# Optimization experiments

Hardware: AMD Instinct MI355X
Metric: run time of the kernel (lower is better)

The kernel has to match this reference:

```python
import jax, jax.numpy as jnp
import numpy as np

N = 32768      # total points (8 clouds x 4096)
B = 8          # clouds in batch
D_IN = 64      # input feature dim
M = 8192       # sampled centers (ratio=0.25)
K = 32         # knn neighbors
R = 0.2        # ball radius
DIMS = [D_IN + 3, 128, 128, 256]  # edge MLP (PointNetConv local_nn)


def setup_inputs() -> dict:
    key = jax.random.key(0)
    ks = jax.random.split(key, 10)
    x = jax.random.normal(ks[0], (N, D_IN), jnp.float32)
    pos = jax.random.uniform(ks[1], (N, 3), jnp.float32)  # unit cube
    batch = jnp.repeat(jnp.arange(B, dtype=jnp.int32), N // B)
    # deterministic stand-in for torch.sort(torch.randperm(N)[:M])
    idx = jnp.sort(jax.random.permutation(ks[2], N)[:M]).astype(jnp.int32)
    params = {}
    for i in range(3):
        fan_in = DIMS[i]
        params[f"W{i+1}"] = jax.random.normal(ks[3 + 2 * i], (DIMS[i], DIMS[i + 1]), jnp.float32) / np.sqrt(fan_in)
        params[f"b{i+1}"] = jnp.zeros((DIMS[i + 1],), jnp.float32)
    return {"x": x, "pos": pos, "batch": batch, "idx": idx, **params}


def _knn_ball(pos, batch, idx, k, r):
    """Batched KNN restricted to same cloud, then radius mask (ball query)."""
    centers = pos[idx]                                   # [M, 3]
    d2 = (jnp.sum(centers ** 2, -1)[:, None]
          + jnp.sum(pos ** 2, -1)[None, :]
          - 2.0 * centers @ pos.T)                       # [M, N]
    same = batch[idx][:, None] == batch[None, :]
    d2 = jnp.where(same, d2, jnp.inf)
    neg_d2, nbr = jax.lax.top_k(-d2, k)                  # [M, K]
    valid = (-neg_d2) <= r * r                           # ball-query radius clip
    return nbr, valid


def reference(x, pos, batch, idx, W1, b1, W2, b2, W3, b3):
    nbr, valid = _knn_ball(pos, batch, idx, K, R)        # [M,K], [M,K]
    centers = pos[idx]                                   # [M, 3]
    rel = pos[nbr] - centers[:, None, :]                 # [M, K, 3]
    feat = jnp.concatenate([x[nbr], rel], axis=-1)       # [M, K, D_IN+3]
    h = jax.nn.relu(feat @ W1 + b1)
    h = jax.nn.relu(h @ W2 + b2)
    h = jax.nn.relu(h @ W3 + b3)                         # [M, K, 256]
    # max aggregation over valid neighbors (scatter-max equivalent)
    h = jnp.where(valid[:, :, None], h, -jnp.inf)
    out = jnp.max(h, axis=1)                             # [M, 256]
    return out, pos[idx], batch[idx]
```

## Files before the change

### kernel.cpp

```cpp
#include <hip/hip_runtime.h>


typedef unsigned short u16;
typedef unsigned int u32;
typedef unsigned long long u64;
typedef __bf16 bf16x8 __attribute__((ext_vector_type(8)));
typedef float floatx4 __attribute__((ext_vector_type(4)));

#define PCLOUD 4096
#define DIN    64
#define MCENT  8192
#define KNBR   32
#define CAP    448

#define OFF_LIST  0
#define OFF_HIST  14336
#define OFF_NBRL  14848
#define OFF_CNT   15360
#define OFF_CEN   15392
#define OFF_BCL   15456

__device__ inline u16 f2bf(float f) {
    u32 b = __float_as_uint(f);
    b += 0x7fffu + ((b >> 16) & 1u);
    return (u16)(b >> 16);
}
__device__ inline u32 cvtpk(float a, float b) {
    u32 r;
    asm("v_cvt_pk_bf16_f32 %0, %1, %2" : "=v"(r) : "v"(a), "v"(b));
    return r;
}
__device__ inline u64 wave_min_u64(u64 v) {
    #pragma unroll
    for (int off = 32; off; off >>= 1) {
        u64 o = __shfl_xor((unsigned long long)v, off);
        if (o < v) v = o;
    }
    return v;
}
__device__ inline u64 d2key(float d2, int j) {
    u32 u = __float_as_uint(d2);
    u = (u & 0x80000000u) ? ~u : (u | 0x80000000u);
    return ((u64)u << 32) | (u32)j;
}
__device__ inline int key_bucket(u64 k) {
    u32 hi = (u32)(k >> 32);
    if (hi < 0x80000000u) return 0;
    float d2 = __uint_as_float(hi & 0x7fffffffu);
    int b = (int)(d2 * 800.0f);
    return b > 31 ? 31 : b;
}

__global__ void prep_kernel(const float* __restrict__ W1, const float* __restrict__ W2,
                            const float* __restrict__ W3, uint4* __restrict__ ws) {
    int t = blockIdx.x * 256 + threadIdx.x;
    int g = t >> 11, r = t & 2047;
    int n = r >> 4, kc = r & 15;
    const float* W; int rs, n0, krows;
    if (g == 0)      { W = W1; rs = 128; n0 = 0;   krows = 67;  }
    else if (g == 1) { W = W2; rs = 128; n0 = 0;   krows = 128; }
    else if (g == 2) { W = W3; rs = 256; n0 = 0;   krows = 128; }
    else             { W = W3; rs = 256; n0 = 128; krows = 128; }
    u16 e[8];
    #pragma unroll
    for (int j = 0; j < 8; j++) {
        int k = kc * 8 + j;
        e[j] = (k < krows) ? f2bf(W[(size_t)k * rs + n0 + n]) : (u16)0;
    }
    ws[(g << 11) + (n << 4) + (kc ^ (n & 7))] = *(const uint4*)e;
}

template <bool WS>
__device__ __forceinline__ void commitW(int s, uint4 ld, uint4* __restrict__ buf, int tid,
                                        const float* __restrict__ W1,
                                        const float* __restrict__ W2,
                                        const float* __restrict__ W3) {
    if constexpr (WS) {
        buf[tid] = ld;
    } else {
        const float* W; int rs, n0, krows;
        if (s < 8)       { W = W1; rs = 128; n0 = s * 16;        krows = 67;  }
        else if (s < 16) { W = W2; rs = 128; n0 = (s - 8) * 16;  krows = 128; }
        else             { W = W3; rs = 256; n0 = (s - 16) * 16; krows = 128; }
        int n = tid >> 4, kc = tid & 15;
        u16 e[8];
        #pragma unroll
        for (int j = 0; j < 8; j++) {
            int k = kc * 8 + j;
            e[j] = (k < krows) ? f2bf(W[(size_t)k * rs + n0 + n]) : (u16)0;
        }
        buf[(n << 4) + (kc ^ (n & 7))] = *(const uint4*)e;
    }
}

__device__ __forceinline__ void push_hit(int c, float d2, int j,
                                         int* acnt, u64* lists) {
    int p = atomicAdd(&acnt[c], 1);
    if (p < CAP) lists[c * CAP + p] = d2key(d2, j);
}

template <bool WS>
__global__ __launch_bounds__(256, 4) void sa_kernel(
    const float* __restrict__ x, const float* __restrict__ pos,
    const int* __restrict__ batch, const int* __restrict__ idx,
    const float* __restrict__ W1, const float* __restrict__ b1,
    const float* __restrict__ W2, const float* __restrict__ b2,
    const float* __restrict__ W3, const float* __restrict__ b3,
    const uint4* __restrict__ ws4, float* __restrict__ out) {
    __shared__ __align__(16) char smem[40960];
    u64*  lists = (u64*)(smem + OFF_LIST);
    u32*  hist  = (u32*)(smem + OFF_HIST);
    int*  nbrl  = (int*)(smem + OFF_NBRL);
    int*  acnt  = (int*)(smem + OFF_CNT);
    int*  cnt2  = (int*)(smem + OFF_CNT + 16);
    float4* cen = (float4*)(smem + OFF_CEN);
    int*  bcls  = (int*)(smem + OFF_BCL);

    int tid = threadIdx.x, w = tid >> 6, l = tid & 63;
    int bid = blockIdx.x;
    int m0 = ((bid & 7) << 10) + ((bid >> 3) << 2);
    int m = m0 + w;
    int ic = idx[m] & (8 * PCLOUD - 1);
    float cx = pos[ic * 3], cy = pos[ic * 3 + 1], cz = pos[ic * 3 + 2];
    float sc = __fadd_rn(__fadd_rn(__fmul_rn(cx, cx), __fmul_rn(cy, cy)), __fmul_rn(cz, cz));
    int bcl = batch[ic] & 7;
    int base = bcl << 12;
    const float R2 = 0.04f;

    if (l == 0) { cen[w] = make_float4(cx, cy, cz, sc); bcls[w] = bcl; }
    if (tid < 4) { acnt[tid] = 0; cnt2[tid] = 0; }
    if (l == 1) {
        float* o1 = out + MCENT * 256;
        o1[m * 3] = cx; o1[m * 3 + 1] = cy; o1[m * 3 + 2] = cz;
        (o1 + MCENT * 3)[m] = (float)bcl;
    }
    __syncthreads();

    bool uni = (bcls[0] == bcls[1]) && (bcls[1] == bcls[2]) && (bcls[2] == bcls[3]);
    if (uni) {
        float4 cA = cen[0], cB = cen[1], cC = cen[2], cD = cen[3];
        int jb = bcls[0] << 12;
        const float4* pb4 = (const float4*)(pos + (size_t)jb * 3);

#define TEST1(CEN, CI, SP, PX, PY, PZ, J) { \
    float dt = __fadd_rn(__fadd_rn(__fmul_rn(CEN.x, PX), __fmul_rn(CEN.y, PY)), __fmul_rn(CEN.z, PZ)); \
    float d2 = __fsub_rn(__fadd_rn(CEN.w, SP), __fmul_rn(2.0f, dt)); \
    if (d2 <= R2) push_hit(CI, d2, J, acnt, lists); }
#define TESTP(PX, PY, PZ, J) { \
    float sp = __fadd_rn(__fadd_rn(__fmul_rn(PX, PX), __fmul_rn(PY, PY)), __fmul_rn(PZ, PZ)); \
    TEST1(cA, 0, sp, PX, PY, PZ, J) \
    TEST1(cB, 1, sp, PX, PY, PZ, J) \
    TEST1(cC, 2, sp, PX, PY, PZ, J) \
    TEST1(cD, 3, sp, PX, PY, PZ, J) }

        #pragma unroll
        for (int it = 0; it < 4; it++) {
            int tq = it * 256 + tid;
            float4 q0 = pb4[tq * 3], q1 = pb4[tq * 3 + 1], q2 = pb4[tq * 3 + 2];
            int j0 = jb + tq * 4;
            TESTP(q0.x, q0.y, q0.z, j0)
            TESTP(q0.w, q1.x, q1.y, j0 + 1)
            TESTP(q1.z, q1.w, q2.x, j0 + 2)
            TESTP(q2.y, q2.z, q2.w, j0 + 3)
        }
#undef TESTP
#undef TEST1
    } else {
        for (int t = l; t < PCLOUD; t += 64) {
            int j = base + t;
            float px = pos[j * 3], py = pos[j * 3 + 1], pz = pos[j * 3 + 2];
            float sp = __fadd_rn(__fadd_rn(__fmul_rn(px, px), __fmul_rn(py, py)), __fmul_rn(pz, pz));
            float dt = __fadd_rn(__fadd_rn(__fmul_rn(cx, px), __fmul_rn(cy, py)), __fmul_rn(cz, pz));
            float d2 = __fsub_rn(__fadd_rn(sc, sp), __fmul_rn(2.0f, dt));
            if (d2 <= R2) push_hit(w, d2, j, acnt, lists);
        }
    }
    __syncthreads();

    int c = acnt[w];
    int nsel = c < KNBR ? c : KNBR;
    u64* mylist = lists + w * CAP;

    int selj = -1;
    if (c <= KNBR) {
        if (l < c) selj = (int)(u32)mylist[l];
    } else if (c <= CAP) {
        u64 kk[7];
        int bk[7];
        if (l < 32) hist[w * 32 + l] = 0;
        #pragma unroll
        for (int i = 0; i < 7; i++) kk[i] = (l + i * 64 < c) ? mylist[l + i * 64] : ~0ull;
        #pragma unroll
        for (int i = 0; i < 7; i++) {
            bk[i] = 32;
            if (kk[i] != ~0ull) {
                bk[i] = key_bucket(kk[i]);
                atomicAdd(&hist[w * 32 + bk[i]], 1u);
            }
        }
        int hv = (l < 32) ? (int)hist[w * 32 + l] : 0;
        #pragma unroll
        for (int off = 1; off <= 16; off <<= 1) {
            int o = __shfl_up(hv, off);
            if (l >= off) hv += o;
        }
        u64 ge = __ballot((l < 32) && (hv >= KNBR));
        int B = __ffsll((unsigned long long)ge) - 1;
        int S = (B == 0) ? 0 : __shfl(hv, B - 1);
        #pragma unroll
        for (int i = 0; i < 7; i++) {
            if (kk[i] != ~0ull) {
                if (bk[i] < B) { int p = atomicAdd(&cnt2[w], 1); nbrl[w * 32 + p] = (int)(u32)kk[i]; }
                if (bk[i] != B) kk[i] = ~0ull;
            }
        }
        int need = KNBR - S;
        u64 last = 0;
        for (int r = 0; r < need; r++) {
            u64 mn = ~0ull;
            #pragma unroll
            for (int i = 0; i < 7; i++) if (kk[i] > last && kk[i] < mn) mn = kk[i];
            mn = wave_min_u64(mn);
            if (l == 0) nbrl[w * 32 + S + r] = (int)(u32)mn;
            last = mn;
        }
        if (l < KNBR) selj = nbrl[w * 32 + l];
    } else {
        u64 last = 0;
        for (int r = 0; r < KNBR; r++) {
            u64 mn = ~0ull;
            for (int t = l; t < PCLOUD; t += 64) {
                int j = base + t;
                float px = pos[j * 3], py = pos[j * 3 + 1], pz = pos[j * 3 + 2];
                float sp = __fadd_rn(__fadd_rn(__fmul_rn(px, px), __fmul_rn(py, py)), __fmul_rn(pz, pz));
                float dt = __fadd_rn(__fadd_rn(__fmul_rn(cx, px), __fmul_rn(cy, py)), __fmul_rn(cz, pz));
                float d2 = __fsub_rn(__fadd_rn(sc, sp), __fmul_rn(2.0f, dt));
                if (d2 <= R2) { u64 kf = d2key(d2, j); if (kf > last && kf < mn) mn = kf; }
            }
            mn = wave_min_u64(mn);
            if (l == r) selj = (int)(u32)mn;
            last = mn;
        }
    }
    __syncthreads();

    uint4* sA4  = (uint4*)smem;
    uint4* sWb0 = (uint4*)(smem + 32768);
    uint4* sWb1 = (uint4*)(smem + 36864);

    uint4 ld = {};
    if constexpr (WS) ld = ws4[tid];

    {
        int h = l & 1, rl = l >> 1;
        int row = w * 32 + rl;
        int j = __shfl(selj, rl);
        int xv = row & 7;
        uint4* dst = sA4 + row * 16;
        uint4 z; z.x = z.y = z.z = z.w = 0;
        if (j >= 0) {
            const float4* sx = (const float4*)(x + (size_t)j * DIN);
            int c0lo = h ? 6 : 0, c0hi = h ? 8 : 6;
            for (int c0 = c0lo; c0 < c0hi; c0++) {
                float4 f0 = sx[c0 * 2], f1 = sx[c0 * 2 + 1];
                uint4 pv;
                pv.x = cvtpk(f0.x, f0.y); pv.y = cvtpk(f0.z, f0.w);
                pv.z = cvtpk(f1.x, f1.y); pv.w = cvtpk(f1.z, f1.w);
                dst[c0 ^ xv] = pv;
            }
            if (h == 1) {
                float rx = pos[j * 3] - cx, ry = pos[j * 3 + 1] - cy, rz = pos[j * 3 + 2] - cz;
                uint4 rc; rc.x = cvtpk(rx, ry); rc.y = cvtpk(rz, 0.0f); rc.z = 0; rc.w = 0;
                dst[8 ^ xv] = rc;
                dst[9 ^ xv] = z; dst[10 ^ xv] = z; dst[11 ^ xv] = z;
            }
        } else {
            int c0lo = h ? 6 : 0, c0hi = h ? 12 : 6;
            for (int c0 = c0lo; c0 < c0hi; c0++) dst[c0 ^ xv] = z;
        }
    }
    commitW<WS>(0, ld, sWb0, tid, W1, W2, W3);
    if constexpr (WS) ld = ws4[256 + tid];
    __syncthreads();

    int m16 = l & 15, quad = l >> 4;
    int r0 = w * 32;
    const floatx4 vzero = {0.f, 0.f, 0.f, 0.f};

    {
        bf16x8 a1[3][2];
        #pragma unroll
        for (int ki = 0; ki < 3; ki++)
            #pragma unroll
            for (int t = 0; t < 2; t++) {
                int row = r0 + t * 16 + m16;
                a1[ki][t] = __builtin_bit_cast(bf16x8, sA4[row * 16 + ((ki * 4 + quad) ^ (row & 7))]);
            }
        #pragma unroll 2
        for (int s = 0; s < 8; s++) {
            uint4* buf  = (s & 1) ? sWb1 : sWb0;
            uint4* nbuf = (s & 1) ? sWb0 : sWb1;
            floatx4 acc[2] = {vzero, vzero};
            #pragma unroll
            for (int ki = 0; ki < 3; ki++) {
                bf16x8 b = __builtin_bit_cast(bf16x8, buf[(m16 << 4) + ((ki * 4 + quad) ^ (m16 & 7))]);
                #pragma unroll
                for (int t = 0; t < 2; t++)
                    acc[t] = __builtin_amdgcn_mfma_f32_16x16x32_bf16(b, a1[ki][t], acc[t], 0, 0, 0);
            }
            float4 bb = ((const float4*)b1)[s * 4 + quad];
            #pragma unroll
            for (int t = 0; t < 2; t++) {
                int rr = r0 + t * 16 + m16;
                uint2 pv;
                pv.x = cvtpk(fmaxf(acc[t][0] + bb.x, 0.f), fmaxf(acc[t][1] + bb.y, 0.f));
                pv.y = cvtpk(fmaxf(acc[t][2] + bb.z, 0.f), fmaxf(acc[t][3] + bb.w, 0.f));
                *(uint2*)(smem + rr * 256 + (((s * 2 + (quad >> 1)) ^ (rr & 7)) << 4) + ((quad & 1) << 3)) = pv;
            }
            commitW<WS>(s + 1, ld, nbuf, tid, W1, W2, W3);
            if constexpr (WS) ld = ws4[(s + 2) * 256 + tid];
            __syncthreads();
        }
    }

    {
        bf16x8 a2[4][2];
        #pragma unroll
        for (int ki = 0; ki < 4; ki++)
            #pragma unroll
            for (int t = 0; t < 2; t++) {
                int row = r0 + t * 16 + m16;
                a2[ki][t] = __builtin_bit_cast(bf16x8, sA4[row * 16 + ((ki * 4 + quad) ^ (row & 7))]);
            }
        #pragma unroll 2
        for (int s = 0; s < 8; s++) {
            uint4* buf  = (s & 1) ? sWb1 : sWb0;
            uint4* nbuf = (s & 1) ? sWb0 : sWb1;
            floatx4 acc[2] = {vzero, vzero};
            #pragma unroll
            for (int ki = 0; ki < 4; ki++) {
                bf16x8 b = __builtin_bit_cast(bf16x8, buf[(m16 << 4) + ((ki * 4 + quad) ^ (m16 & 7))]);
                #pragma unroll
                for (int t = 0; t < 2; t++)
                    acc[t] = __builtin_amdgcn_mfma_f32_16x16x32_bf16(b, a2[ki][t], acc[t], 0, 0, 0);
            }
            float4 bb = ((const float4*)b2)[s * 4 + quad];
            #pragma unroll
            for (int t = 0; t < 2; t++) {
                int rr = r0 + t * 16 + m16;
                uint2 pv;
                pv.x = cvtpk(fmaxf(acc[t][0] + bb.x, 0.f), fmaxf(acc[t][1] + bb.y, 0.f));
                pv.y = cvtpk(fmaxf(acc[t][2] + bb.z, 0.f), fmaxf(acc[t][3] + bb.w, 0.f));
                *(uint2*)(smem + rr * 256 + (((s * 2 + (quad >> 1)) ^ (rr & 7)) << 4) + ((quad & 1) << 3)) = pv;
            }
            commitW<WS>(s + 9, ld, nbuf, tid, W1, W2, W3);
            if constexpr (WS) ld = ws4[(s + 10) * 256 + tid];
            __syncthreads();
        }
    }

    {
        bf16x8 a3[4][2];
        #pragma unroll
        for (int ki = 0; ki < 4; ki++)
            #pragma unroll
            for (int t = 0; t < 2; t++) {
                int row = r0 + t * 16 + m16;
                a3[ki][t] = __builtin_bit_cast(bf16x8, sA4[row * 16 + ((ki * 4 + quad) ^ (row & 7))]);
            }
        #pragma unroll 2
        for (int s = 0; s < 16; s++) {
            uint4* buf  = (s & 1) ? sWb1 : sWb0;
            uint4* nbuf = (s & 1) ? sWb0 : sWb1;
            floatx4 acc[2] = {vzero, vzero};
            #pragma unroll
            for (int ki = 0; ki < 4; ki++) {
                bf16x8 b = __builtin_bit_cast(bf16x8, buf[(m16 << 4) + ((ki * 4 + quad) ^ (m16 & 7))]);
                #pragma unroll
                for (int t = 0; t < 2; t++)
                    acc[t] = __builtin_amdgcn_mfma_f32_16x16x32_bf16(a3[ki][t], b, acc[t], 0, 0, 0);
            }
            int col = s * 16 + m16;
            float bias = b3[col];
            float mv = 0.0f;
            #pragma unroll
            for (int t = 0; t < 2; t++)
                #pragma unroll
                for (int i = 0; i < 4; i++) {
                    int k = t * 16 + quad * 4 + i;
                    float v = fmaxf(acc[t][i] + bias, 0.0f);
                    if (k < nsel) mv = fmaxf(mv, v);
                }
            mv = fmaxf(mv, __shfl_xor(mv, 16));
            mv = fmaxf(mv, __shfl_xor(mv, 32));
            if (quad == 0) out[(m0 + w) * 256 + col] = mv;
            if (s < 15) {
                commitW<WS>(s + 17, ld, nbuf, tid, W1, W2, W3);
                if constexpr (WS) { if (s < 14) ld = ws4[(s + 18) * 256 + tid]; }
                __syncthreads();
            }
        }
    }
}

extern "C" void kernel_launch(void* const* d_in, const int* in_sizes, int n_in,
                              void* d_out, int out_size, void* d_ws, size_t ws_size,
                              hipStream_t stream) {
    const float* x     = (const float*)d_in[0];
    const float* pos   = (const float*)d_in[1];
    const int*   batch = (const int*)d_in[2];
    const int*   idx   = (const int*)d_in[3];
    const float* W1    = (const float*)d_in[4];
    const float* b1    = (const float*)d_in[5];
    const float* W2    = (const float*)d_in[6];
    const float* b2    = (const float*)d_in[7];
    const float* W3    = (const float*)d_in[8];
    const float* b3    = (const float*)d_in[9];
    float* out = (float*)d_out;
    uint4* ws4 = (uint4*)d_ws;

    if (ws_size >= 131072) {
        hipLaunchKernelGGL(prep_kernel, dim3(32), dim3(256), 0, stream, W1, W2, W3, ws4);
        hipLaunchKernelGGL((sa_kernel<true>), dim3(MCENT / 4), dim3(256), 0, stream,
                           x, pos, batch, idx, W1, b1, W2, b2, W3, b3, ws4, out);
    } else {
        hipLaunchKernelGGL((sa_kernel<false>), dim3(MCENT / 4), dim3(256), 0, stream,
                           x, pos, batch, idx, W1, b1, W2, b2, W3, b3, ws4, out);
    }
}
```

Before: 152.1 us.

## Stream weights in 32-column slabs and prefetch first slab during KNN

Weight staging buffers are doubled so each pipeline stage covers 32 output columns instead of 16, which halves the number of barrier-separated stages across the three MLP layers. The first weight slab is loaded and committed to shared memory before the neighbor search, so its latency overlaps the KNN phase. MFMA sections are wrapped in s_setprio raises. Shared memory grows to 48 KB and launch bounds drop from 4 to 3 blocks per CU, trading occupancy for fewer syncs.

Result: slower. 170.3 us (+11.9%).

```diff
diff --git a/kernel.cpp b/kernel.cpp
--- a/kernel.cpp
+++ b/kernel.cpp
@@ -71,25 +71,31 @@
 }
 
 template <bool WS>
-__device__ __forceinline__ void commitW(int s, uint4 ld, uint4* __restrict__ buf, int tid,
-                                        const float* __restrict__ W1,
-                                        const float* __restrict__ W2,
-                                        const float* __restrict__ W3) {
+__device__ __forceinline__ void commitW32(int g, uint4 ld0, uint4 ld1,
+                                          uint4* __restrict__ buf, int tid,
+                                          const float* __restrict__ W1,
+                                          const float* __restrict__ W2,
+                                          const float* __restrict__ W3) {
     if constexpr (WS) {
-        buf[tid] = ld;
+        buf[tid] = ld0;
+        buf[256 + tid] = ld1;
     } else {
-        const float* W; int rs, n0, krows;
-        if (s < 8)       { W = W1; rs = 128; n0 = s * 16;        krows = 67;  }
-        else if (s < 16) { W = W2; rs = 128; n0 = (s - 8) * 16;  krows = 128; }
-        else             { W = W3; rs = 256; n0 = (s - 16) * 16; krows = 128; }
-        int n = tid >> 4, kc = tid & 15;
-        u16 e[8];
-        #pragma unroll
-        for (int j = 0; j < 8; j++) {
-            int k = kc * 8 + j;
-            e[j] = (k < krows) ? f2bf(W[(size_t)k * rs + n0 + n]) : (u16)0;
-        }
-        buf[(n << 4) + (kc ^ (n & 7))] = *(const uint4*)e;
+        #pragma unroll
+        for (int h = 0; h < 2; h++) {
+            int b = g * 2 + h;
+            const float* W; int rs, n0, krows;
+            if (b < 8)       { W = W1; rs = 128; n0 = b * 16;        krows = 67;  }
+            else if (b < 16) { W = W2; rs = 128; n0 = (b - 8) * 16;  krows = 128; }
+            else             { W = W3; rs = 256; n0 = (b - 16) * 16; krows = 128; }
+            int n = tid >> 4, kc = tid & 15;
+            u16 e[8];
+            #pragma unroll
+            for (int j = 0; j < 8; j++) {
+                int k = kc * 8 + j;
+                e[j] = (k < krows) ? f2bf(W[(size_t)k * rs + n0 + n]) : (u16)0;
+            }
+            buf[h * 256 + (n << 4) + (kc ^ (n & 7))] = *(const uint4*)e;
+        }
     }
 }
 
@@ -100,14 +106,14 @@
 }
 
 template <bool WS>
-__global__ __launch_bounds__(256, 4) void sa_kernel(
+__global__ __launch_bounds__(256, 3) void sa_kernel(
     const float* __restrict__ x, const float* __restrict__ pos,
     const int* __restrict__ batch, const int* __restrict__ idx,
     const float* __restrict__ W1, const float* __restrict__ b1,
     const float* __restrict__ W2, const float* __restrict__ b2,
     const float* __restrict__ W3, const float* __restrict__ b3,
     const uint4* __restrict__ ws4, float* __restrict__ out) {
-    __shared__ __align__(16) char smem[40960];
+    __shared__ __align__(16) char smem[49152];
     u64*  lists = (u64*)(smem + OFF_LIST);
     u32*  hist  = (u32*)(smem + OFF_HIST);
     int*  nbrl  = (int*)(smem + OFF_NBRL);
@@ -116,7 +122,14 @@
     float4* cen = (float4*)(smem + OFF_CEN);
     int*  bcls  = (int*)(smem + OFF_BCL);
 
+    uint4* sA4  = (uint4*)smem;
+    uint4* sWb0 = (uint4*)(smem + 32768);
+    uint4* sWb1 = (uint4*)(smem + 40960);
+
     int tid = threadIdx.x, w = tid >> 6, l = tid & 63;
+    uint4 ld0 = {}, ld1 = {};
+    if constexpr (WS) { ld0 = ws4[tid]; ld1 = ws4[256 + tid]; }
+
     int bid = blockIdx.x;
     int m0 = ((bid & 7) << 10) + ((bid >> 3) << 2);
     int m = m0 + w;
@@ -134,6 +147,7 @@
         o1[m * 3] = cx; o1[m * 3 + 1] = cy; o1[m * 3 + 2] = cz;
         (o1 + MCENT * 3)[m] = (float)bcl;
     }
+    commitW32<WS>(0, ld0, ld1, sWb0, tid, W1, W2, W3);
     __syncthreads();
 
     bool uni = (bcls[0] == bcls[1]) && (bcls[1] == bcls[2]) && (bcls[2] == bcls[3]);
@@ -244,12 +258,7 @@
     }
     __syncthreads();
 
-    uint4* sA4  = (uint4*)smem;
-    uint4* sWb0 = (uint4*)(smem + 32768);
-    uint4* sWb1 = (uint4*)(smem + 36864);
-
-    uint4 ld = {};
-    if constexpr (WS) ld = ws4[tid];
+    if constexpr (WS) { ld0 = ws4[512 + tid]; ld1 = ws4[768 + tid]; }
 
     {
         int h = l & 1, rl = l >> 1;
@@ -279,8 +288,6 @@
             for (int c0 = c0lo; c0 < c0hi; c0++) dst[c0 ^ xv] = z;
         }
     }
-    commitW<WS>(0, ld, sWb0, tid, W1, W2, W3);
-    if constexpr (WS) ld = ws4[256 + tid];
     __syncthreads();
 
     int m16 = l & 15, quad = l >> 4;
@@ -295,108 +302,139 @@
             for (int t = 0; t < 2; t++) {
                 int row = r0 + t * 16 + m16;
                 a1[ki][t] = __builtin_bit_cast(bf16x8, sA4[row * 16 + ((ki * 4 + quad) ^ (row & 7))]);
+            }
+        #pragma unroll 2
+        for (int s = 0; s < 4; s++) {
+            uint4* buf  = (s & 1) ? sWb1 : sWb0;
+            uint4* nbuf = (s & 1) ? sWb0 : sWb1;
+            floatx4 acc[2][2] = {{vzero, vzero}, {vzero, vzero}};
+            __builtin_amdgcn_s_setprio(1);
+            #pragma unroll
+            for (int ki = 0; ki < 3; ki++) {
+                int cb = ki * 4 + quad;
+                #pragma unroll
+                for (int cc = 0; cc < 2; cc++) {
+                    bf16x8 b = __builtin_bit_cast(bf16x8, buf[cc * 256 + (m16 << 4) + (cb ^ (m16 & 7))]);
+                    #pragma unroll
+                    for (int t = 0; t < 2; t++)
+                        acc[t][cc] = __builtin_amdgcn_mfma_f32_16x16x32_bf16(b, a1[ki][t], acc[t][cc], 0, 0, 0);
+                }
+            }
+            __builtin_amdgcn_s_setprio(0);
+            #pragma unroll
+            for (int t = 0; t < 2; t++) {
+                int rr = r0 + t * 16 + m16;
+                #pragma unroll
+                for (int cc = 0; cc < 2; cc++) {
+                    float4 bb = ((const float4*)b1)[s * 8 + cc * 4 + quad];
+                    uint2 pv;
+                    pv.x = cvtpk(fmaxf(acc[t][cc][0] + bb.x, 0.f), fmaxf(acc[t][cc][1] + bb.y, 0.f));
+                    pv.y = cvtpk(fmaxf(acc[t][cc][2] + bb.z, 0.f), fmaxf(acc[t][cc][3] + bb.w, 0.f));
+                    *(uint2*)(smem + rr * 256 + (((s * 4 + cc * 2 + (quad >> 1)) ^ (rr & 7)) << 4)
+                              + ((quad & 1) << 3)) = pv;
+                }
+            }
+            commitW32<WS>(s + 1, ld0, ld1, nbuf, tid, W1, W2, W3);
+            if constexpr (WS) { ld0 = ws4[(s + 2) * 512 + tid]; ld1 = ws4[(s + 2) * 512 + 256 + tid]; }
+            __syncthreads();
+        }
+    }
+
+    {
+        bf16x8 a2[4][2];
+        #pragma unroll
+        for (int ki = 0; ki < 4; ki++)
+            #pragma unroll
+            for (int t = 0; t < 2; t++) {
+                int row = r0 + t * 16 + m16;
+                a2[ki][t] = __builtin_bit_cast(bf16x8, sA4[row * 16 + ((ki * 4 + quad) ^ (row & 7))]);
+            }
+        #pragma unroll 2
+        for (int s = 0; s < 4; s++) {
+            uint4* buf  = (s & 1) ? sWb1 : sWb0;
+            uint4* nbuf = (s & 1) ? sWb0 : sWb1;
+            floatx4 acc[2][2] = {{vzero, vzero}, {vzero, vzero}};
+            __builtin_amdgcn_s_setprio(1);
+            #pragma unroll
+            for (int ki = 0; ki < 4; ki++) {
+                int cb = ki * 4 + quad;
+                #pragma unroll
+                for (int cc = 0; cc < 2; cc++) {
+                    bf16x8 b = __builtin_bit_cast(bf16x8, buf[cc * 256 + (m16 << 4) + (cb ^ (m16 & 7))]);
+                    #pragma unroll
+                    for (int t = 0; t < 2; t++)
+                        acc[t][cc] = __builtin_amdgcn_mfma_f32_16x16x32_bf16(b, a2[ki][t], acc[t][cc], 0, 0, 0);
+                }
+            }
+            __builtin_amdgcn_s_setprio(0);
+            #pragma unroll
+            for (int t = 0; t < 2; t++) {
+                int rr = r0 + t * 16 + m16;
+                #pragma unroll
+                for (int cc = 0; cc < 2; cc++) {
+                    float4 bb = ((const float4*)b2)[s * 8 + cc * 4 + quad];
+                    uint2 pv;
+                    pv.x = cvtpk(fmaxf(acc[t][cc][0] + bb.x, 0.f), fmaxf(acc[t][cc][1] + bb.y, 0.f));
+                    pv.y = cvtpk(fmaxf(acc[t][cc][2] + bb.z, 0.f), fmaxf(acc[t][cc][3] + bb.w, 0.f));
+                    *(uint2*)(smem + rr * 256 + (((s * 4 + cc * 2 + (quad >> 1)) ^ (rr & 7)) << 4)
+                              + ((quad & 1) << 3)) = pv;
+                }
+            }
+            commitW32<WS>(s + 5, ld0, ld1, nbuf, tid, W1, W2, W3);
+            if constexpr (WS) { ld0 = ws4[(s + 6) * 512 + tid]; ld1 = ws4[(s + 6) * 512 + 256 + tid]; }
+            __syncthreads();
+        }
+    }
+
+    {
+        bf16x8 a3[4][2];
+        #pragma unroll
+        for (int ki = 0; ki < 4; ki++)
+            #pragma unroll
+            for (int t = 0; t < 2; t++) {
+                int row = r0 + t * 16 + m16;
+                a3[ki][t] = __builtin_bit_cast(bf16x8, sA4[row * 16 + ((ki * 4 + quad) ^ (row & 7))]);
             }
         #pragma unroll 2
         for (int s = 0; s < 8; s++) {
             uint4* buf  = (s & 1) ? sWb1 : sWb0;
             uint4* nbuf = (s & 1) ? sWb0 : sWb1;
-            floatx4 acc[2] = {vzero, vzero};
-            #pragma unroll
-            for (int ki = 0; ki < 3; ki++) {
-                bf16x8 b = __builtin_bit_cast(bf16x8, buf[(m16 << 4) + ((ki * 4 + quad) ^ (m16 & 7))]);
+            floatx4 acc[2][2] = {{vzero, vzero}, {vzero, vzero}};
+            __builtin_amdgcn_s_setprio(1);
+            #pragma unroll
+            for (int ki = 0; ki < 4; ki++) {
+                int cb = ki * 4 + quad;
+                #pragma unroll
+                for (int cc = 0; cc < 2; cc++) {
+                    bf16x8 b = __builtin_bit_cast(bf16x8, buf[cc * 256 + (m16 << 4) + (cb ^ (m16 & 7))]);
+                    #pragma unroll
+                    for (int t = 0; t < 2; t++)
+                        acc[t][cc] = __builtin_amdgcn_mfma_f32_16x16x32_bf16(a3[ki][t], b, acc[t][cc], 0, 0, 0);
+                }
+            }
+            __builtin_amdgcn_s_setprio(0);
+            #pragma unroll
+            for (int cc = 0; cc < 2; cc++) {
+                int col = s * 32 + cc * 16 + m16;
+                float bias = b3[col];
+                float mv = 0.0f;
                 #pragma unroll
                 for (int t = 0; t < 2; t++)
-                    acc[t] = __builtin_amdgcn_mfma_f32_16x16x32_bf16(b, a1[ki][t], acc[t], 0, 0, 0);
-            }
-            float4 bb = ((const float4*)b1)[s * 4 + quad];
-            #pragma unroll
-            for (int t = 0; t < 2; t++) {
-                int rr = r0 + t * 16 + m16;
-                uint2 pv;
-                pv.x = cvtpk(fmaxf(acc[t][0] + bb.x, 0.f), fmaxf(acc[t][1] + bb.y, 0.f));
-                pv.y = cvtpk(fmaxf(acc[t][2] + bb.z, 0.f), fmaxf(acc[t][3] + bb.w, 0.f));
-                *(uint2*)(smem + rr * 256 + (((s * 2 + (quad >> 1)) ^ (rr & 7)) << 4) + ((quad & 1) << 3)) = pv;
-            }
-            commitW<WS>(s + 1, ld, nbuf, tid, W1, W2, W3);
-            if constexpr (WS) ld = ws4[(s + 2) * 256 + tid];
-            __syncthreads();
-        }
-    }
-
-    {
-        bf16x8 a2[4][2];
-        #pragma unroll
-        for (int ki = 0; ki < 4; ki++)
-            #pragma unroll
-            for (int t = 0; t < 2; t++) {
-                int row = r0 + t * 16 + m16;
-                a2[ki][t] = __builtin_bit_cast(bf16x8, sA4[row * 16 + ((ki * 4 + quad) ^ (row & 7))]);
-            }
-        #pragma unroll 2
-        for (int s = 0; s < 8; s++) {
-            uint4* buf  = (s & 1) ? sWb1 : sWb0;
-            uint4* nbuf = (s & 1) ? sWb0 : sWb1;
-            floatx4 acc[2] = {vzero, vzero};
-            #pragma unroll
-            for (int ki = 0; ki < 4; ki++) {
-                bf16x8 b = __builtin_bit_cast(bf16x8, buf[(m16 << 4) + ((ki * 4 + quad) ^ (m16 & 7))]);
-                #pragma unroll
-                for (int t = 0; t < 2; t++)
-                    acc[t] = __builtin_amdgcn_mfma_f32_16x16x32_bf16(b, a2[ki][t], acc[t], 0, 0, 0);
-            }
-            float4 bb = ((const float4*)b2)[s * 4 + quad];
-            #pragma unroll
-            for (int t = 0; t < 2; t++) {
-                int rr = r0 + t * 16 + m16;
-                uint2 pv;
-                pv.x = cvtpk(fmaxf(acc[t][0] + bb.x, 0.f), fmaxf(acc[t][1] + bb.y, 0.f));
-                pv.y = cvtpk(fmaxf(acc[t][2] + bb.z, 0.f), fmaxf(acc[t][3] + bb.w, 0.f));
-                *(uint2*)(smem + rr * 256 + (((s * 2 + (quad >> 1)) ^ (rr & 7)) << 4) + ((quad & 1) << 3)) = pv;
-            }
-            commitW<WS>(s + 9, ld, nbuf, tid, W1, W2, W3);
-            if constexpr (WS) ld = ws4[(s + 10) * 256 + tid];
-            __syncthreads();
-        }
-    }
-
-    {
-        bf16x8 a3[4][2];
-        #pragma unroll
-        for (int ki = 0; ki < 4; ki++)
-            #pragma unroll
-            for (int t = 0; t < 2; t++) {
-                int row = r0 + t * 16 + m16;
-                a3[ki][t] = __builtin_bit_cast(bf16x8, sA4[row * 16 + ((ki * 4 + quad) ^ (row & 7))]);
-            }
-        #pragma unroll 2
-        for (int s = 0; s < 16; s++) {
-            uint4* buf  = (s & 1) ? sWb1 : sWb0;
-            uint4* nbuf = (s & 1) ? sWb0 : sWb1;
-            floatx4 acc[2] = {vzero, vzero};
-            #pragma unroll
-            for (int ki = 0; ki < 4; ki++) {
-                bf16x8 b = __builtin_bit_cast(bf16x8, buf[(m16 << 4) + ((ki * 4 + quad) ^ (m16 & 7))]);
-                #pragma unroll
-                for (int t = 0; t < 2; t++)
-                    acc[t] = __builtin_amdgcn_mfma_f32_16x16x32_bf16(a3[ki][t], b, acc[t], 0, 0, 0);
-            }
-            int col = s * 16 + m16;
-            float bias = b3[col];
-            float mv = 0.0f;
-            #pragma unroll
-            for (int t = 0; t < 2; t++)
-                #pragma unroll
-                for (int i = 0; i < 4; i++) {
-                    int k = t * 16 + quad * 4 + i;
-                    float v = fmaxf(acc[t][i] + bias, 0.0f);
-                    if (k < nsel) mv = fmaxf(mv, v);
-                }
-            mv = fmaxf(mv, __shfl_xor(mv, 16));
-            mv = fmaxf(mv, __shfl_xor(mv, 32));
-            if (quad == 0) out[(m0 + w) * 256 + col] = mv;
-            if (s < 15) {
-                commitW<WS>(s + 17, ld, nbuf, tid, W1, W2, W3);
-                if constexpr (WS) { if (s < 14) ld = ws4[(s + 18) * 256 + tid]; }
+                    #pragma unroll
+                    for (int i = 0; i < 4; i++) {
+                        int k = t * 16 + quad * 4 + i;
+                        float v = fmaxf(acc[t][cc][i] + bias, 0.0f);
+                        if (k < nsel) mv = fmaxf(mv, v);
+                    }
+                mv = fmaxf(mv, __shfl_xor(mv, 16));
+                mv = fmaxf(mv, __shfl_xor(mv, 32));
+                if (quad == 0) out[(m0 + w) * 256 + col] = mv;
+            }
+            if (s < 7) {
+                commitW32<WS>(s + 9, ld0, ld1, nbuf, tid, W1, W2, W3);
+                if constexpr (WS) {
+                    if (s < 6) { ld0 = ws4[(s + 10) * 512 + tid]; ld1 = ws4[(s + 10) * 512 + 256 + tid]; }
+                }
                 __syncthreads();
             }
         }
```

## Load MLP weight fragments directly into registers and drop block barriers

Applied to the files above, without the earlier changes.

Replaces the LDS double-buffered weight staging, written by all 256 threads and fenced by __syncthreads every step, with per-wave register prefetch. Each wave now reads its B fragments straight from the pre-swizzled workspace, or converts them from fp32 in the fallback path, one column block ahead. This removes the block-wide barriers between MLP steps and cuts shared memory from 40 KB to 32 KB. MFMA sections are wrapped in s_setprio. The cost is that every wave fetches the full weight set from cache, so L2 traffic rises about fourfold, and full unrolling adds register pressure.

Measured after the change: 163.7 us. +7.6%, slower.

```diff
diff --git a/kernel.cpp b/kernel.cpp
--- a/kernel.cpp
+++ b/kernel.cpp
@@ -70,27 +70,18 @@
     ws[(g << 11) + (n << 4) + (kc ^ (n & 7))] = *(const uint4*)e;
 }
 
-template <bool WS>
-__device__ __forceinline__ void commitW(int s, uint4 ld, uint4* __restrict__ buf, int tid,
-                                        const float* __restrict__ W1,
-                                        const float* __restrict__ W2,
-                                        const float* __restrict__ W3) {
-    if constexpr (WS) {
-        buf[tid] = ld;
-    } else {
-        const float* W; int rs, n0, krows;
-        if (s < 8)       { W = W1; rs = 128; n0 = s * 16;        krows = 67;  }
-        else if (s < 16) { W = W2; rs = 128; n0 = (s - 8) * 16;  krows = 128; }
-        else             { W = W3; rs = 256; n0 = (s - 16) * 16; krows = 128; }
-        int n = tid >> 4, kc = tid & 15;
-        u16 e[8];
-        #pragma unroll
-        for (int j = 0; j < 8; j++) {
-            int k = kc * 8 + j;
-            e[j] = (k < krows) ? f2bf(W[(size_t)k * rs + n0 + n]) : (u16)0;
-        }
-        buf[(n << 4) + (kc ^ (n & 7))] = *(const uint4*)e;
-    }
+__device__ __forceinline__ uint4 ldB_ws(const uint4* __restrict__ ws4, int blk, int cb, int m16) {
+    return ws4[blk * 256 + (m16 << 4) + (cb ^ (m16 & 7))];
+}
+__device__ __forceinline__ uint4 ldB_fb(const float* __restrict__ W, int rs, int col,
+                                        int cb, int krows) {
+    u16 e[8];
+    #pragma unroll
+    for (int j = 0; j < 8; j++) {
+        int k = cb * 8 + j;
+        e[j] = (k < krows) ? f2bf(W[(size_t)k * rs + col]) : (u16)0;
+    }
+    return *(const uint4*)e;
 }
 
 __device__ __forceinline__ void push_hit(int c, float d2, int j,
@@ -107,7 +98,7 @@
     const float* __restrict__ W2, const float* __restrict__ b2,
     const float* __restrict__ W3, const float* __restrict__ b3,
     const uint4* __restrict__ ws4, float* __restrict__ out) {
-    __shared__ __align__(16) char smem[40960];
+    __shared__ __align__(16) char smem[32768];
     u64*  lists = (u64*)(smem + OFF_LIST);
     u32*  hist  = (u32*)(smem + OFF_HIST);
     int*  nbrl  = (int*)(smem + OFF_NBRL);
@@ -115,6 +106,7 @@
     int*  cnt2  = (int*)(smem + OFF_CNT + 16);
     float4* cen = (float4*)(smem + OFF_CEN);
     int*  bcls  = (int*)(smem + OFF_BCL);
+    uint4* sA4  = (uint4*)smem;
 
     int tid = threadIdx.x, w = tid >> 6, l = tid & 63;
     int bid = blockIdx.x;
@@ -243,13 +235,6 @@
         }
     }
     __syncthreads();
-
-    uint4* sA4  = (uint4*)smem;
-    uint4* sWb0 = (uint4*)(smem + 32768);
-    uint4* sWb1 = (uint4*)(smem + 36864);
-
-    uint4 ld = {};
-    if constexpr (WS) ld = ws4[tid];
 
     {
         int h = l & 1, rl = l >> 1;
@@ -279,14 +264,14 @@
             for (int c0 = c0lo; c0 < c0hi; c0++) dst[c0 ^ xv] = z;
         }
     }
-    commitW<WS>(0, ld, sWb0, tid, W1, W2, W3);
-    if constexpr (WS) ld = ws4[256 + tid];
-    __syncthreads();
 
     int m16 = l & 15, quad = l >> 4;
     int r0 = w * 32;
     const floatx4 vzero = {0.f, 0.f, 0.f, 0.f};
 
+#define LDB(BLK, CB, W, RS, COL, KR) \
+    (WS ? ldB_ws(ws4, (BLK), (CB), m16) : ldB_fb((W), (RS), (COL), (CB), (KR)))
+
     {
         bf16x8 a1[3][2];
         #pragma unroll
@@ -296,18 +281,27 @@
                 int row = r0 + t * 16 + m16;
                 a1[ki][t] = __builtin_bit_cast(bf16x8, sA4[row * 16 + ((ki * 4 + quad) ^ (row & 7))]);
             }
-        #pragma unroll 2
+        uint4 bc[3];
+        #pragma unroll
+        for (int ki = 0; ki < 3; ki++) bc[ki] = LDB(0, ki * 4 + quad, W1, 128, m16, 67);
+        #pragma unroll
         for (int s = 0; s < 8; s++) {
-            uint4* buf  = (s & 1) ? sWb1 : sWb0;
-            uint4* nbuf = (s & 1) ? sWb0 : sWb1;
+            uint4 bn[3];
+            if (s < 7) {
+                #pragma unroll
+                for (int ki = 0; ki < 3; ki++)
+                    bn[ki] = LDB(s + 1, ki * 4 + quad, W1, 128, (s + 1) * 16 + m16, 67);
+            }
             floatx4 acc[2] = {vzero, vzero};
+            __builtin_amdgcn_s_setprio(1);
             #pragma unroll
             for (int ki = 0; ki < 3; ki++) {
-                bf16x8 b = __builtin_bit_cast(bf16x8, buf[(m16 << 4) + ((ki * 4 + quad) ^ (m16 & 7))]);
+                bf16x8 b = __builtin_bit_cast(bf16x8, bc[ki]);
                 #pragma unroll
                 for (int t = 0; t < 2; t++)
                     acc[t] = __builtin_amdgcn_mfma_f32_16x16x32_bf16(b, a1[ki][t], acc[t], 0, 0, 0);
             }
+            __builtin_amdgcn_s_setprio(0);
             float4 bb = ((const float4*)b1)[s * 4 + quad];
             #pragma unroll
             for (int t = 0; t < 2; t++) {
@@ -317,9 +311,10 @@
                 pv.y = cvtpk(fmaxf(acc[t][2] + bb.z, 0.f), fmaxf(acc[t][3] + bb.w, 0.f));
                 *(uint2*)(smem + rr * 256 + (((s * 2 + (quad >> 1)) ^ (rr & 7)) << 4) + ((quad & 1) << 3)) = pv;
             }
-            commitW<WS>(s + 1, ld, nbuf, tid, W1, W2, W3);
-            if constexpr (WS) ld = ws4[(s + 2) * 256 + tid];
-            __syncthreads();
+            if (s < 7) {
+                #pragma unroll
+                for (int ki = 0; ki < 3; ki++) bc[ki] = bn[ki];
+            }
         }
     }
 
@@ -332,18 +327,27 @@
                 int row = r0 + t * 16 + m16;
                 a2[ki][t] = __builtin_bit_cast(bf16x8, sA4[row * 16 + ((ki * 4 + quad) ^ (row & 7))]);
             }
-        #pragma unroll 2
+        uint4 bc[4];
+        #pragma unroll
+        for (int ki = 0; ki < 4; ki++) bc[ki] = LDB(8, ki * 4 + quad, W2, 128, m16, 128);
+        #pragma unroll
         for (int s = 0; s < 8; s++) {
-            uint4* buf  = (s & 1) ? sWb1 : sWb0;
-            uint4* nbuf = (s & 1) ? sWb0 : sWb1;
+            uint4 bn[4];
+            if (s < 7) {
+                #pragma unroll
+                for (int ki = 0; ki < 4; ki++)
+                    bn[ki] = LDB(9 + s, ki * 4 + quad, W2, 128, (s + 1) * 16 + m16, 128);
+            }
             floatx4 acc[2] = {vzero, vzero};
+            __builtin_amdgcn_s_setprio(1);
             #pragma unroll
             for (int ki = 0; ki < 4; ki++) {
-                bf16x8 b = __builtin_bit_cast(bf16x8, buf[(m16 << 4) + ((ki * 4 + quad) ^ (m16 & 7))]);
+                bf16x8 b = __builtin_bit_cast(bf16x8, bc[ki]);
                 #pragma unroll
                 for (int t = 0; t < 2; t++)
                     acc[t] = __builtin_amdgcn_mfma_f32_16x16x32_bf16(b, a2[ki][t], acc[t], 0, 0, 0);
             }
+            __builtin_amdgcn_s_setprio(0);
             float4 bb = ((const float4*)b2)[s * 4 + quad];
             #pragma unroll
             for (int t = 0; t < 2; t++) {
@@ -353,9 +357,10 @@
                 pv.y = cvtpk(fmaxf(acc[t][2] + bb.z, 0.f), fmaxf(acc[t][3] + bb.w, 0.f));
                 *(uint2*)(smem + rr * 256 + (((s * 2 + (quad >> 1)) ^ (rr & 7)) << 4) + ((quad & 1) << 3)) = pv;
             }
-            commitW<WS>(s + 9, ld, nbuf, tid, W1, W2, W3);
-            if constexpr (WS) ld = ws4[(s + 10) * 256 + tid];
-            __syncthreads();
+            if (s < 7) {
+                #pragma unroll
+                for (int ki = 0; ki < 4; ki++) bc[ki] = bn[ki];
+            }
         }
     }
 
@@ -368,18 +373,27 @@
                 int row = r0 + t * 16 + m16;
                 a3[ki][t] = __builtin_bit_cast(bf16x8, sA4[row * 16 + ((ki * 4 + quad) ^ (row & 7))]);
             }
-        #pragma unroll 2
+        uint4 bc[4];
+        #pragma unroll
+        for (int ki = 0; ki < 4; ki++) bc[ki] = LDB(16, ki * 4 + quad, W3, 256, m16, 128);
+        #pragma unroll
         for (int s = 0; s < 16; s++) {
-            uint4* buf  = (s & 1) ? sWb1 : sWb0;
-            uint4* nbuf = (s & 1) ? sWb0 : sWb1;
+            uint4 bn[4];
+            if (s < 15) {
+                #pragma unroll
+                for (int ki = 0; ki < 4; ki++)
+                    bn[ki] = LDB(17 + s, ki * 4 + quad, W3, 256, (s + 1) * 16 + m16, 128);
+            }
             floatx4 acc[2] = {vzero, vzero};
+            __builtin_amdgcn_s_setprio(1);
             #pragma unroll
             for (int ki = 0; ki < 4; ki++) {
-                bf16x8 b = __builtin_bit_cast(bf16x8, buf[(m16 << 4) + ((ki * 4 + quad) ^ (m16 & 7))]);
+                bf16x8 b = __builtin_bit_cast(bf16x8, bc[ki]);
                 #pragma unroll
                 for (int t = 0; t < 2; t++)
                     acc[t] = __builtin_amdgcn_mfma_f32_16x16x32_bf16(a3[ki][t], b, acc[t], 0, 0, 0);
             }
+            __builtin_amdgcn_s_setprio(0);
             int col = s * 16 + m16;
             float bias = b3[col];
             float mv = 0.0f;
@@ -395,12 +409,12 @@
             mv = fmaxf(mv, __shfl_xor(mv, 32));
             if (quad == 0) out[(m0 + w) * 256 + col] = mv;
             if (s < 15) {
-                commitW<WS>(s + 17, ld, nbuf, tid, W1, W2, W3);
-                if constexpr (WS) { if (s < 14) ld = ws4[(s + 18) * 256 + tid]; }
-                __syncthreads();
-            }
-        }
-    }
+                #pragma unroll
+                for (int ki = 0; ki < 4; ki++) bc[ki] = bn[ki];
+            }
+        }
+    }
+#undef LDB
 }
 
 extern "C" void kernel_launch(void* const* d_in, const int* in_sizes, int n_in,
```

## Simplify distance math, pad neighbors by duplication, and hoist bias out of max

Applied to the files above, without the earlier changes.

Distance tests now use FMA chains with precomputed -2*center and store raw non-negative float bits as sort keys, with a sqrt-based bucket mapping. Empty neighbor slots are filled with the first selected neighbor, so the gather no longer branches on invalid indices and the final max needs no per-row validity mask. Bias and ReLU are applied once after the max reduction instead of per element. s_setprio is raised around the MFMA blocks. Duplicate padding relies on at least one neighbor always existing (the center itself), and FMA rounding can change borderline radius and tie decisions compared with the reference.

Result: slower. 155.2 us (+2.0%).

```diff
diff --git a/kernel.cpp b/kernel.cpp
--- a/kernel.cpp
+++ b/kernel.cpp
@@ -38,17 +38,12 @@
     }
     return v;
 }
-__device__ inline u64 d2key(float d2, int j) {
-    u32 u = __float_as_uint(d2);
-    u = (u & 0x80000000u) ? ~u : (u | 0x80000000u);
-    return ((u64)u << 32) | (u32)j;
-}
 __device__ inline int key_bucket(u64 k) {
-    u32 hi = (u32)(k >> 32);
-    if (hi < 0x80000000u) return 0;
-    float d2 = __uint_as_float(hi & 0x7fffffffu);
-    int b = (int)(d2 * 800.0f);
-    return b > 31 ? 31 : b;
+    float d2 = __uint_as_float((u32)(k >> 32));
+    float t = d2 * 25.0f;
+    float b = 32.0f * t * __builtin_sqrtf(t);
+    int bi = (int)b;
+    return bi > 31 ? 31 : bi;
 }
 
 __global__ void prep_kernel(const float* __restrict__ W1, const float* __restrict__ W2,
@@ -96,7 +91,8 @@
 __device__ __forceinline__ void push_hit(int c, float d2, int j,
                                          int* acnt, u64* lists) {
     int p = atomicAdd(&acnt[c], 1);
-    if (p < CAP) lists[c * CAP + p] = d2key(d2, j);
+    u64 key = ((u64)__float_as_uint(fmaxf(d2, 0.0f)) << 32) | (u32)j;
+    if (p < CAP) lists[c * CAP + p] = key;
 }
 
 template <bool WS>
@@ -115,6 +111,9 @@
     int*  cnt2  = (int*)(smem + OFF_CNT + 16);
     float4* cen = (float4*)(smem + OFF_CEN);
     int*  bcls  = (int*)(smem + OFF_BCL);
+    uint4* sA4  = (uint4*)smem;
+    uint4* sWb0 = (uint4*)(smem + 32768);
+    uint4* sWb1 = (uint4*)(smem + 36864);
 
     int tid = threadIdx.x, w = tid >> 6, l = tid & 63;
     int bid = blockIdx.x;
@@ -139,19 +138,23 @@
     bool uni = (bcls[0] == bcls[1]) && (bcls[1] == bcls[2]) && (bcls[2] == bcls[3]);
     if (uni) {
         float4 cA = cen[0], cB = cen[1], cC = cen[2], cD = cen[3];
+        float nAx = -2.0f * cA.x, nAy = -2.0f * cA.y, nAz = -2.0f * cA.z;
+        float nBx = -2.0f * cB.x, nBy = -2.0f * cB.y, nBz = -2.0f * cB.z;
+        float nCx = -2.0f * cC.x, nCy = -2.0f * cC.y, nCz = -2.0f * cC.z;
+        float nDx = -2.0f * cD.x, nDy = -2.0f * cD.y, nDz = -2.0f * cD.z;
         int jb = bcls[0] << 12;
         const float4* pb4 = (const float4*)(pos + (size_t)jb * 3);
 
-#define TEST1(CEN, CI, SP, PX, PY, PZ, J) { \
-    float dt = __fadd_rn(__fadd_rn(__fmul_rn(CEN.x, PX), __fmul_rn(CEN.y, PY)), __fmul_rn(CEN.z, PZ)); \
-    float d2 = __fsub_rn(__fadd_rn(CEN.w, SP), __fmul_rn(2.0f, dt)); \
+#define TEST1(NX, NY, NZ, SW, CI, SP, PX, PY, PZ, J) { \
+    float d2 = __builtin_fmaf((NX), (PX), __builtin_fmaf((NY), (PY), \
+               __builtin_fmaf((NZ), (PZ), (SW) + (SP)))); \
     if (d2 <= R2) push_hit(CI, d2, J, acnt, lists); }
 #define TESTP(PX, PY, PZ, J) { \
-    float sp = __fadd_rn(__fadd_rn(__fmul_rn(PX, PX), __fmul_rn(PY, PY)), __fmul_rn(PZ, PZ)); \
-    TEST1(cA, 0, sp, PX, PY, PZ, J) \
-    TEST1(cB, 1, sp, PX, PY, PZ, J) \
-    TEST1(cC, 2, sp, PX, PY, PZ, J) \
-    TEST1(cD, 3, sp, PX, PY, PZ, J) }
+    float sp = __builtin_fmaf((PX), (PX), __builtin_fmaf((PY), (PY), (PZ) * (PZ))); \
+    TEST1(nAx, nAy, nAz, cA.w, 0, sp, PX, PY, PZ, J) \
+    TEST1(nBx, nBy, nBz, cB.w, 1, sp, PX, PY, PZ, J) \
+    TEST1(nCx, nCy, nCz, cC.w, 2, sp, PX, PY, PZ, J) \
+    TEST1(nDx, nDy, nDz, cD.w, 3, sp, PX, PY, PZ, J) }
 
         #pragma unroll
         for (int it = 0; it < 4; it++) {
@@ -166,19 +169,19 @@
 #undef TESTP
 #undef TEST1
     } else {
+        float nx = -2.0f * cx, ny = -2.0f * cy, nz = -2.0f * cz;
         for (int t = l; t < PCLOUD; t += 64) {
             int j = base + t;
             float px = pos[j * 3], py = pos[j * 3 + 1], pz = pos[j * 3 + 2];
-            float sp = __fadd_rn(__fadd_rn(__fmul_rn(px, px), __fmul_rn(py, py)), __fmul_rn(pz, pz));
-            float dt = __fadd_rn(__fadd_rn(__fmul_rn(cx, px), __fmul_rn(cy, py)), __fmul_rn(cz, pz));
-            float d2 = __fsub_rn(__fadd_rn(sc, sp), __fmul_rn(2.0f, dt));
+            float sp = __builtin_fmaf(px, px, __builtin_fmaf(py, py, pz * pz));
+            float d2 = __builtin_fmaf(nx, px, __builtin_fmaf(ny, py,
+                       __builtin_fmaf(nz, pz, sc + sp)));
             if (d2 <= R2) push_hit(w, d2, j, acnt, lists);
         }
     }
     __syncthreads();
 
     int c = acnt[w];
-    int nsel = c < KNBR ? c : KNBR;
     u64* mylist = lists + w * CAP;
 
     int selj = -1;
@@ -226,27 +229,31 @@
         }
         if (l < KNBR) selj = nbrl[w * 32 + l];
     } else {
+        float nx = -2.0f * cx, ny = -2.0f * cy, nz = -2.0f * cz;
         u64 last = 0;
         for (int r = 0; r < KNBR; r++) {
             u64 mn = ~0ull;
             for (int t = l; t < PCLOUD; t += 64) {
                 int j = base + t;
                 float px = pos[j * 3], py = pos[j * 3 + 1], pz = pos[j * 3 + 2];
-                float sp = __fadd_rn(__fadd_rn(__fmul_rn(px, px), __fmul_rn(py, py)), __fmul_rn(pz, pz));
-                float dt = __fadd_rn(__fadd_rn(__fmul_rn(cx, px), __fmul_rn(cy, py)), __fmul_rn(cz, pz));
-                float d2 = __fsub_rn(__fadd_rn(sc, sp), __fmul_rn(2.0f, dt));
-                if (d2 <= R2) { u64 kf = d2key(d2, j); if (kf > last && kf < mn) mn = kf; }
+                float sp = __builtin_fmaf(px, px, __builtin_fmaf(py, py, pz * pz));
+                float d2 = __builtin_fmaf(nx, px, __builtin_fmaf(ny, py,
+                           __builtin_fmaf(nz, pz, sc + sp)));
+                if (d2 <= R2) {
+                    u64 kf = ((u64)__float_as_uint(fmaxf(d2, 0.0f)) << 32) | (u32)j;
+                    if (kf > last && kf < mn) mn = kf;
+                }
             }
             mn = wave_min_u64(mn);
             if (l == r) selj = (int)(u32)mn;
             last = mn;
         }
     }
+    {
+        int s0 = __shfl(selj, 0);
+        if (selj < 0) selj = s0;
+    }
     __syncthreads();
-
-    uint4* sA4  = (uint4*)smem;
-    uint4* sWb0 = (uint4*)(smem + 32768);
-    uint4* sWb1 = (uint4*)(smem + 36864);
 
     uint4 ld = {};
     if constexpr (WS) ld = ws4[tid];
@@ -257,26 +264,38 @@
         int j = __shfl(selj, rl);
         int xv = row & 7;
         uint4* dst = sA4 + row * 16;
-        uint4 z; z.x = z.y = z.z = z.w = 0;
-        if (j >= 0) {
-            const float4* sx = (const float4*)(x + (size_t)j * DIN);
-            int c0lo = h ? 6 : 0, c0hi = h ? 8 : 6;
-            for (int c0 = c0lo; c0 < c0hi; c0++) {
-                float4 f0 = sx[c0 * 2], f1 = sx[c0 * 2 + 1];
+        const float4* sx = (const float4*)(x + (size_t)j * DIN);
+        if (h == 0) {
+            float4 f[12];
+            #pragma unroll
+            for (int i = 0; i < 12; i++) f[i] = sx[i];
+            #pragma unroll
+            for (int c0 = 0; c0 < 6; c0++) {
                 uint4 pv;
-                pv.x = cvtpk(f0.x, f0.y); pv.y = cvtpk(f0.z, f0.w);
-                pv.z = cvtpk(f1.x, f1.y); pv.w = cvtpk(f1.z, f1.w);
+                pv.x = cvtpk(f[c0 * 2].x, f[c0 * 2].y);
+                pv.y = cvtpk(f[c0 * 2].z, f[c0 * 2].w);
+                pv.z = cvtpk(f[c0 * 2 + 1].x, f[c0 * 2 + 1].y);
+                pv.w = cvtpk(f[c0 * 2 + 1].z, f[c0 * 2 + 1].w);
                 dst[c0 ^ xv] = pv;
             }
-            if (h == 1) {
-                float rx = pos[j * 3] - cx, ry = pos[j * 3 + 1] - cy, rz = pos[j * 3 + 2] - cz;
-                uint4 rc; rc.x = cvtpk(rx, ry); rc.y = cvtpk(rz, 0.0f); rc.z = 0; rc.w = 0;
-                dst[8 ^ xv] = rc;
-                dst[9 ^ xv] = z; dst[10 ^ xv] = z; dst[11 ^ xv] = z;
-            }
         } else {
-            int c0lo = h ? 6 : 0, c0hi = h ? 12 : 6;
-            for (int c0 = c0lo; c0 < c0hi; c0++) dst[c0 ^ xv] = z;
+            uint4 z; z.x = z.y = z.z = z.w = 0;
+            float4 f[4];
+            #pragma unroll
+            for (int i = 0; i < 4; i++) f[i] = sx[12 + i];
+            float rx = pos[j * 3] - cx, ry = pos[j * 3 + 1] - cy, rz = pos[j * 3 + 2] - cz;
+            #pragma unroll
+            for (int c0 = 0; c0 < 2; c0++) {
+                uint4 pv;
+                pv.x = cvtpk(f[c0 * 2].x, f[c0 * 2].y);
+                pv.y = cvtpk(f[c0 * 2].z, f[c0 * 2].w);
+                pv.z = cvtpk(f[c0 * 2 + 1].x, f[c0 * 2 + 1].y);
+                pv.w = cvtpk(f[c0 * 2 + 1].z, f[c0 * 2 + 1].w);
+                dst[(6 + c0) ^ xv] = pv;
+            }
+            uint4 rc; rc.x = cvtpk(rx, ry); rc.y = cvtpk(rz, 0.0f); rc.z = 0; rc.w = 0;
+            dst[8 ^ xv] = rc;
+            dst[9 ^ xv] = z; dst[10 ^ xv] = z; dst[11 ^ xv] = z;
         }
     }
     commitW<WS>(0, ld, sWb0, tid, W1, W2, W3);
@@ -301,6 +320,7 @@
             uint4* buf  = (s & 1) ? sWb1 : sWb0;
             uint4* nbuf = (s & 1) ? sWb0 : sWb1;
             floatx4 acc[2] = {vzero, vzero};
+            __builtin_amdgcn_s_setprio(1);
             #pragma unroll
             for (int ki = 0; ki < 3; ki++) {
                 bf16x8 b = __builtin_bit_cast(bf16x8, buf[(m16 << 4) + ((ki * 4 + quad) ^ (m16 & 7))]);
@@ -308,6 +328,7 @@
                 for (int t = 0; t < 2; t++)
                     acc[t] = __builtin_amdgcn_mfma_f32_16x16x32_bf16(b, a1[ki][t], acc[t], 0, 0, 0);
             }
+            __builtin_amdgcn_s_setprio(0);
             float4 bb = ((const float4*)b1)[s * 4 + quad];
             #pragma unroll
             for (int t = 0; t < 2; t++) {
@@ -337,6 +358,7 @@
             uint4* buf  = (s & 1) ? sWb1 : sWb0;
             uint4* nbuf = (s & 1) ? sWb0 : sWb1;
             floatx4 acc[2] = {vzero, vzero};
+            __builtin_amdgcn_s_setprio(1);
             #pragma unroll
             for (int ki = 0; ki < 4; ki++) {
                 bf16x8 b = __builtin_bit_cast(bf16x8, buf[(m16 << 4) + ((ki * 4 + quad) ^ (m16 & 7))]);
@@ -344,6 +366,7 @@
                 for (int t = 0; t < 2; t++)
                     acc[t] = __builtin_amdgcn_mfma_f32_16x16x32_bf16(b, a2[ki][t], acc[t], 0, 0, 0);
             }
+            __builtin_amdgcn_s_setprio(0);
             float4 bb = ((const float4*)b2)[s * 4 + quad];
             #pragma unroll
             for (int t = 0; t < 2; t++) {
@@ -373,6 +396,7 @@
             uint4* buf  = (s & 1) ? sWb1 : sWb0;
             uint4* nbuf = (s & 1) ? sWb0 : sWb1;
             floatx4 acc[2] = {vzero, vzero};
+            __builtin_amdgcn_s_setprio(1);
             #pragma unroll
             for (int ki = 0; ki < 4; ki++) {
                 bf16x8 b = __builtin_bit_cast(bf16x8, buf[(m16 << 4) + ((ki * 4 + quad) ^ (m16 & 7))]);
@@ -380,19 +404,13 @@
                 for (int t = 0; t < 2; t++)
                     acc[t] = __builtin_amdgcn_mfma_f32_16x16x32_bf16(a3[ki][t], b, acc[t], 0, 0, 0);
             }
+            __builtin_amdgcn_s_setprio(0);
             int col = s * 16 + m16;
-            float bias = b3[col];
-            float mv = 0.0f;
-            #pragma unroll
-            for (int t = 0; t < 2; t++)
-                #pragma unroll
-                for (int i = 0; i < 4; i++) {
-                    int k = t * 16 + quad * 4 + i;
-                    float v = fmaxf(acc[t][i] + bias, 0.0f);
-                    if (k < nsel) mv = fmaxf(mv, v);
-                }
+            float mv = fmaxf(fmaxf(fmaxf(acc[0][0], acc[0][1]), fmaxf(acc[0][2], acc[0][3])),
+                             fmaxf(fmaxf(acc[1][0], acc[1][1]), fmaxf(acc[1][2], acc[1][3])));
             mv = fmaxf(mv, __shfl_xor(mv, 16));
             mv = fmaxf(mv, __shfl_xor(mv, 32));
+            mv = fmaxf(mv + b3[col], 0.0f);
             if (quad == 0) out[(m0 + w) * 256 + col] = mv;
             if (s < 15) {
                 commitW<WS>(s + 17, ld, nbuf, tid, W1, W2, W3);
```
